# Performance work log

Hardware: AMD Instinct MI355X
Metric: run time of the kernel (lower is better)

The kernel has to match this reference:

```python
import jax, jax.numpy as jnp
import numpy as np

N_NODES = 100000
NUM_FEATURES = 64
HIDDEN = 128
OUT_CONV2 = 100


def gcn_conv(x, W, b, src, dst, n):
    """PyG GCNConv: add self-loops, symmetric degree norm, scatter-add."""
    x = x @ W  # [N, out]
    loop = jnp.arange(n, dtype=src.dtype)
    src2 = jnp.concatenate([src, loop])  # [E+N]
    dst2 = jnp.concatenate([dst, loop])
    deg = jax.ops.segment_sum(jnp.ones_like(dst2, dtype=x.dtype), dst2, num_segments=n)
    dinv = jnp.where(deg > 0, deg ** -0.5, 0.0)
    norm = dinv[src2] * dinv[dst2]  # [E+N]
    msg = x[src2] * norm[:, None]  # gather + scale
    out = jax.ops.segment_sum(msg, dst2, num_segments=n)  # scatter-add
    return out + b


def setup_inputs() -> dict:
    key = jax.random.key(0)
    ks = jax.random.split(key, 8)
    E = 1600000
    x = jax.random.normal(ks[0], (N_NODES, NUM_FEATURES), dtype=jnp.float32)
    edge_index = jax.random.randint(ks[1], (2, E), 0, N_NODES, dtype=jnp.int64)
    # Glorot-style init for GCNConv weights, zeros bias (PyG defaults)
    s1 = (6.0 / (NUM_FEATURES + HIDDEN)) ** 0.5
    W1 = jax.random.uniform(ks[2], (NUM_FEATURES, HIDDEN), minval=-s1, maxval=s1, dtype=jnp.float32)
    b1 = jnp.zeros((HIDDEN,), dtype=jnp.float32)
    s2 = (6.0 / (HIDDEN + OUT_CONV2)) ** 0.5
    W2 = jax.random.uniform(ks[3], (HIDDEN, OUT_CONV2), minval=-s2, maxval=s2, dtype=jnp.float32)
    b2 = jnp.zeros((OUT_CONV2,), dtype=jnp.float32)
    sl = (1.0 / OUT_CONV2) ** 0.5
    Wl = jax.random.uniform(ks[4], (OUT_CONV2, 1), minval=-sl, maxval=sl, dtype=jnp.float32)
    bl = jax.random.uniform(ks[5], (1,), minval=-sl, maxval=sl, dtype=jnp.float32)
    return {"x": x, "edge_index": edge_index, "W1": W1, "b1": b1,
            "W2": W2, "b2": b2, "Wl": Wl, "bl": bl}


def reference(x, edge_index, W1, b1, W2, b2, Wl, bl):
    src, dst = edge_index[0], edge_index[1]
    h = gcn_conv(x, W1, b1, src, dst, N_NODES)
    h = jax.nn.relu(h)
    # F.dropout with training=False (eval/inference) is identity
    h = gcn_conv(h, W2, b2, src, dst, N_NODES)
    return h @ Wl + bl  # [N, 1]
```

## Files before the change

### kernel.cpp

```cpp
#include <hip/hip_runtime.h>
#include <hip/hip_fp16.h>


#define N_NODES 100000
#define F_IN 64
#define HID 128
#define OUT2 100
#define BSHIFT 6
#define BNODES 64
#define NBUCKETS ((N_NODES + BNODES - 1) / BNODES)
#define SCAP 1408
#define ACHUNK 4096
#define NB_PAD 2048
#define SENTB 0xFFFFu
#define SENTE 0xFFFFFFFFu
#define TSHIFT 13
#define NTILES 13
#define RSTRIDE 77
#define ZROW N_NODES
#define YSCALE 4096.0f
#define YINV   (1.0f / 4096.0f)
#define ZSCALE 8192.0f
#define ZINV   (1.0f / 8192.0f)

typedef _Float16 half8 __attribute__((ext_vector_type(8)));
typedef float f32x4 __attribute__((ext_vector_type(4)));

static __device__ __forceinline__ half8 as_half8(uint4 u) {
    union { uint4 u; half8 h; } x; x.u = u; return x.h;
}

__global__ __launch_bounds__(256) void partA_kernel(
    const int* __restrict__ src, const int* __restrict__ dst,
    int* __restrict__ bcur, unsigned int* __restrict__ ebuf, int E, int nchunks,
    const float* __restrict__ W1, const float* __restrict__ W2,
    const float* __restrict__ b2, const float* __restrict__ Wl,
    const float* __restrict__ bl,
    float* __restrict__ v, float* __restrict__ c, uint4* __restrict__ Wpk,
    int* __restrict__ yzero) {
    int t = threadIdx.x;
    if ((int)blockIdx.x >= nchunks) {
        int pb = (int)blockIdx.x - nchunks;
        if (pb < 8) {
            int idx = pb * 256 + t;
            int lane2 = idx & 63;
            int kf    = (idx >> 6) & 1;
            int cb    = (idx >> 7) & 7;
            int part  = (idx >> 10) & 1;
            union { uint4 u; unsigned short s[8]; } pk;
            #pragma unroll
            for (int j = 0; j < 8; ++j) {
                int k    = kf * 32 + (lane2 >> 4) * 8 + j;
                int colg = cb * 16 + (lane2 & 15);
                float w = W1[k * HID + colg];
                __half h = __float2half_rn(w);
                if (part) h = __float2half_rn(w - __half2float(h));
                pk.s[j] = __half_as_ushort(h);
            }
            Wpk[idx] = pk.u;
        } else {
            if (t < HID) {
                float acc = 0.f;
                for (int k = 0; k < OUT2; ++k) acc += W2[t * OUT2 + k] * Wl[k];
                v[t] = acc;
            } else if (t == HID) {
                float acc = bl[0];
                for (int k = 0; k < OUT2; ++k) acc += b2[k] * Wl[k];
                *c = acc;
            }
            if (t < 128) yzero[t] = 0;
        }
        return;
    }
    __shared__ unsigned int stage[ACHUNK];
    __shared__ unsigned short sb[ACHUNK];
    __shared__ int hist[NB_PAD];
    __shared__ int ocnt[NB_PAD];
    __shared__ int gbase[NB_PAD];
    __shared__ int cnt2[NB_PAD];
    int base = blockIdx.x * ACHUNK;
    int total = E - base; if (total > ACHUNK) total = ACHUNK;

    #pragma unroll
    for (int i = 0; i < 8; ++i) { hist[t + i * 256] = 0; cnt2[t + i * 256] = 0; }
    __syncthreads();

    unsigned int pe[16];
    unsigned short bk[16];
    #pragma unroll
    for (int k = 0; k < 16; ++k) {
        int e = base + k * 256 + t;
        if (e < E) {
            int s = src[e], d = dst[e];
            pe[k] = ((unsigned int)s << BSHIFT) | (unsigned int)(d & (BNODES - 1));
            bk[k] = (unsigned short)(d >> BSHIFT);
            atomicAdd(&hist[bk[k]], 1);
        } else {
            bk[k] = SENTB;
        }
    }
    __syncthreads();
    #pragma unroll
    for (int i = 0; i < 8; ++i) ocnt[t + i * 256] = hist[t + i * 256];
    __syncthreads();
    for (int off = 1; off < NB_PAD; off <<= 1) {
        int v8[8];
        #pragma unroll
        for (int i = 0; i < 8; ++i) {
            int p = t + i * 256;
            v8[i] = (p >= off) ? hist[p - off] : 0;
        }
        __syncthreads();
        #pragma unroll
        for (int i = 0; i < 8; ++i) hist[t + i * 256] += v8[i];
        __syncthreads();
    }
    #pragma unroll
    for (int i = 0; i < 8; ++i) {
        int b = (t + i * 256 + blockIdx.x * 131) & (NB_PAD - 1);
        int cc = ocnt[b];
        if (cc > 0 && b < NBUCKETS)
            gbase[b] = b * SCAP + atomicAdd(&bcur[b], cc);
    }
    __syncthreads();
    #pragma unroll
    for (int k = 0; k < 16; ++k) {
        if (bk[k] != SENTB) {
            int b = bk[k];
            int pos = (hist[b] - ocnt[b]) + atomicAdd(&cnt2[b], 1);
            stage[pos] = pe[k];
            sb[pos] = (unsigned short)b;
        }
    }
    __syncthreads();
    #pragma unroll
    for (int k = 0; k < 16; ++k) {
        int idx = k * 256 + t;
        if (idx < total) {
            int b = sb[idx];
            int lo = hist[b] - ocnt[b];
            ebuf[gbase[b] + (idx - lo)] = stage[idx];
        }
    }
}

__global__ __launch_bounds__(256) void partB_kernel(
    const int* __restrict__ bcur, unsigned int* __restrict__ csr,
    float* __restrict__ dinv,
    const float4* __restrict__ x4, uint2* __restrict__ y2, int n) {
    __shared__ int lcnt[BNODES];
    __shared__ float sdinv[BNODES];
    __shared__ int tcnt[16];
    __shared__ int tcur[16];
    __shared__ unsigned int sbuf[SCAP];
    int b = blockIdx.x, t = threadIdx.x;
    int node0 = b << BSHIFT;
    int nlocal = min(BNODES, n - node0);
    int base = b * SCAP;
    int cnt = bcur[b];
    if (t < BNODES) lcnt[t] = 0;
    if (t < 16) tcnt[t] = 0;
    __syncthreads();
    unsigned int er[6];
    #pragma unroll
    for (int k = 0; k < 6; ++k) {
        int idx = k * 256 + t;
        er[k] = (idx < cnt) ? csr[base + idx] : SENTE;
        if (er[k] != SENTE) {
            atomicAdd(&lcnt[er[k] & (BNODES - 1)], 1);
            atomicAdd(&tcnt[er[k] >> (BSHIFT + TSHIFT)], 1);
        }
    }
    __syncthreads();
    if (t < BNODES) {
        float sd = rsqrtf((float)lcnt[t] + 1.0f);
        sdinv[t] = sd;
        if (t < nlocal) dinv[node0 + t] = sd;
    }
    if (t == 0) {
        int s = 0;
        #pragma unroll
        for (int i = 0; i < NTILES; ++i) { tcur[i] = s; s += tcnt[i]; }
    }
    __syncthreads();
    #pragma unroll
    for (int k = 0; k < 6; ++k) {
        unsigned int e = er[k];
        if (e != SENTE) {
            int p = atomicAdd(&tcur[e >> (BSHIFT + TSHIFT)], 1);
            sbuf[p] = e;
        }
    }
    __syncthreads();
    for (int idx = t; idx < cnt; idx += 256) csr[base + idx] = sbuf[idx];
    for (int i = t; i < nlocal * 16; i += 256) {
        int nl = i >> 4;
        int gi = (node0 + nl) * 16 + (i & 15);
        float sc = sdinv[nl] * YSCALE;
        float4 xv = x4[gi];
        int a0 = __float2int_rn(xv.x * sc);
        int a1 = __float2int_rn(xv.y * sc);
        int a2 = __float2int_rn(xv.z * sc);
        int a3 = __float2int_rn(xv.w * sc);
        uint2 pk;
        pk.x = ((unsigned int)a0 & 0xFFFFu) | ((unsigned int)a1 << 16);
        pk.y = ((unsigned int)a2 & 0xFFFFu) | ((unsigned int)a3 << 16);
        y2[gi] = pk;
    }
}

#define F1_ISSUE(EE, U, DL)                                            \
    _Pragma("unroll")                                                  \
    for (int g = 0; g < 8; ++g) {                                      \
        unsigned int e_ = __shfl((EE), g * 8 + q, 64);                 \
        int srow_ = (e_ != SENTE) ? (int)(e_ >> BSHIFT) : ZROW;        \
        DL[g] = (int)(e_ & (BNODES - 1));                              \
        U[g] = y4[srow_ * 8 + col];                                    \
    }

#define F1_CONSUME(U, DL)                                              \
    _Pragma("unroll")                                                  \
    for (int g = 0; g < 8; ++g) {                                      \
        int* rowp_ = &acci[DL[g] * RSTRIDE + col * 9];                 \
        const int* up_ = (const int*)&U[g];                            \
        _Pragma("unroll")                                              \
        for (int j = 0; j < 4; ++j) {                                  \
            int d_ = up_[j];                                           \
            atomicAdd(&rowp_[2 * j],     (d_ << 16) >> 16);            \
            atomicAdd(&rowp_[2 * j + 1], d_ >> 16);                    \
        }                                                              \
    }

__global__ __launch_bounds__(256, 6) void fused1_kernel(
    const int4* __restrict__ y4, const short* __restrict__ yh,
    const unsigned int* __restrict__ csr, const int* __restrict__ bcur,
    const float* __restrict__ dinv, const uint4* __restrict__ Wpk,
    const float* __restrict__ b1, const float* __restrict__ v,
    float* __restrict__ zz, int n) {
    __shared__ int acci[BNODES * RSTRIDE];
    int t = threadIdx.x;
    int lane = t & 63, wave = t >> 6;
    int q = lane >> 3, col = lane & 7;
    int b = blockIdx.x;
    int node0 = b << BSHIFT;
    int nlocal = min(BNODES, n - node0);
    int base = b * SCAP;
    int cnt = bcur[b];

    for (int r = wave; r < BNODES; r += 4) {
        int vv = 0;
        if (r < nlocal) vv = (int)yh[(node0 + r) * 64 + lane];
        acci[r * RSTRIDE + q * 9 + col] = vv;
    }
    __syncthreads();

    int nr = (cnt + 255) >> 8;
    int lpos = wave * 64 + lane;
    unsigned int ee = (lpos < cnt) ? csr[base + lpos] : SENTE;
    for (int r = 0; r < nr; ++r) {
        int pn = lpos + (r + 1) * 256;
        unsigned int een = (pn < cnt) ? csr[base + pn] : SENTE;
        int4 u[8]; int dl[8];
        F1_ISSUE(ee, u, dl);
        F1_CONSUME(u, dl);
        ee = een;
    }
    __syncthreads();

    int mm = lane & 15, kq = lane >> 4;
    int st = wave;
    int row = st * 16 + mm;
    float dis = ((row < nlocal) ? dinv[node0 + row] : 0.f) * YINV;
    const int* ap = &acci[row * RSTRIDE];
    half8 A0, A1;
    #pragma unroll
    for (int j = 0; j < 8; ++j) {
        A0[j] = (_Float16)(dis * (float)ap[kq * 9 + j]);
        A1[j] = (_Float16)(dis * (float)ap[(4 + kq) * 9 + j]);
    }
    f32x4 acc[8];
    #pragma unroll
    for (int cb = 0; cb < 8; ++cb) acc[cb] = (f32x4){0.f, 0.f, 0.f, 0.f};
    #pragma unroll
    for (int cb = 0; cb < 8; ++cb) {
        half8 bh0 = as_half8(Wpk[(cb * 2 + 0) * 64 + lane]);
        half8 bh1 = as_half8(Wpk[(cb * 2 + 1) * 64 + lane]);
        half8 bl0 = as_half8(Wpk[1024 + (cb * 2 + 0) * 64 + lane]);
        half8 bl1 = as_half8(Wpk[1024 + (cb * 2 + 1) * 64 + lane]);
        acc[cb] = __builtin_amdgcn_mfma_f32_16x16x32_f16(A0, bh0, acc[cb], 0, 0, 0);
        acc[cb] = __builtin_amdgcn_mfma_f32_16x16x32_f16(A1, bh1, acc[cb], 0, 0, 0);
        acc[cb] = __builtin_amdgcn_mfma_f32_16x16x32_f16(A0, bl0, acc[cb], 0, 0, 0);
        acc[cb] = __builtin_amdgcn_mfma_f32_16x16x32_f16(A1, bl1, acc[cb], 0, 0, 0);
    }
    float zp[4] = {0.f, 0.f, 0.f, 0.f};
    #pragma unroll
    for (int cb = 0; cb < 8; ++cb) {
        int colg = cb * 16 + mm;
        float bb1 = b1[colg], vv = v[colg];
        #pragma unroll
        for (int rr = 0; rr < 4; ++rr) {
            float h = acc[cb][rr] + bb1;
            h = fmaxf(h, 0.f);
            zp[rr] += h * vv;
        }
    }
    #pragma unroll
    for (int off = 1; off < 16; off <<= 1) {
        #pragma unroll
        for (int rr = 0; rr < 4; ++rr) zp[rr] += __shfl_xor(zp[rr], off, 64);
    }
    if (mm == 0) {
        int nb = st * 16 + kq * 4;
        #pragma unroll
        for (int rr = 0; rr < 4; ++rr)
            if (nb + rr < nlocal)
                zz[node0 + nb + rr] = dinv[node0 + nb + rr] * zp[rr];
    }
}

__global__ __launch_bounds__(256) void out_kernel(
    const int* __restrict__ bcur, const unsigned int* __restrict__ csr,
    const float* __restrict__ dinv, const float* __restrict__ zz,
    const float* __restrict__ c, float* __restrict__ out, int n) {
    __shared__ int acc2[BNODES];
    int b = blockIdx.x, t = threadIdx.x;
    int node0 = b << BSHIFT;
    int nlocal = min(BNODES, n - node0);
    int base = b * SCAP;
    int cnt = bcur[b];
    if (t < BNODES) acc2[t] = 0;
    __syncthreads();
    for (int idx = t; idx < cnt; idx += 256) {
        unsigned int e = csr[base + idx];
        float z = zz[e >> BSHIFT];
        atomicAdd(&acc2[e & (BNODES - 1)], __float2int_rn(z * ZSCALE));
    }
    __syncthreads();
    if (t < nlocal) {
        int node = node0 + t;
        out[node] = c[0] + dinv[node] * ((float)acc2[t] * ZINV + zz[node]);
    }
}

extern "C" void kernel_launch(void* const* d_in, const int* in_sizes, int n_in,
                              void* d_out, int out_size, void* d_ws, size_t ws_size,
                              hipStream_t stream) {
    const float* x  = (const float*)d_in[0];
    const int*   ei = (const int*)d_in[1];
    const float* W1 = (const float*)d_in[2];
    const float* b1 = (const float*)d_in[3];
    const float* W2 = (const float*)d_in[4];
    const float* b2 = (const float*)d_in[5];
    const float* Wl = (const float*)d_in[6];
    const float* bl = (const float*)d_in[7];
    float* out = (float*)d_out;

    int E = in_sizes[1] / 2;
    const int* src = ei;
    const int* dst = ei + E;

    float* ws      = (float*)d_ws;
    float* dinv    = ws;
    float* zz      = dinv + N_NODES;
    float* v       = zz + N_NODES;
    float* c       = v + HID;
    int*   bcur    = (int*)(c + 4);
    int*   csr     = bcur + NB_PAD;
    uint4* Wpk     = (uint4*)(csr + (size_t)NBUCKETS * SCAP);
    short* y       = (short*)((float*)Wpk + 8192);

    int nchunks = (E + ACHUNK - 1) / ACHUNK;

    hipMemsetAsync(bcur, 0, NBUCKETS * sizeof(int), stream);
    partA_kernel<<<nchunks + 9, 256, 0, stream>>>(
        src, dst, bcur, (unsigned int*)csr, E, nchunks,
        W1, W2, b2, Wl, bl, v, c, Wpk, (int*)(y + (size_t)ZROW * 64));
    partB_kernel<<<NBUCKETS, 256, 0, stream>>>(
        bcur, (unsigned int*)csr, dinv, (const float4*)x, (uint2*)y, N_NODES);
    fused1_kernel<<<NBUCKETS, 256, 0, stream>>>(
        (const int4*)y, (const short*)y, (const unsigned int*)csr,
        bcur, dinv, Wpk, b1, v, zz, N_NODES);
    out_kernel<<<NBUCKETS, 256, 0, stream>>>(
        bcur, (const unsigned int*)csr, dinv, zz, c, out, N_NODES);
}
```

Measured before the change: 179.2 us.

## Use two-level block scan in partA and sort edges by (tile, dst) in partB

```diff
diff --git a/kernel.cpp b/kernel.cpp
--- a/kernel.cpp
+++ b/kernel.cpp
@@ -16,6 +16,7 @@
 #define SENTE 0xFFFFFFFFu
 #define TSHIFT 13
 #define NTILES 13
+#define NKEY_PAD 1024
 #define RSTRIDE 77
 #define ZROW N_NODES
 #define YSCALE 4096.0f
@@ -78,6 +79,7 @@
     __shared__ int ocnt[NB_PAD];
     __shared__ int gbase[NB_PAD];
     __shared__ int cnt2[NB_PAD];
+    __shared__ int tsum[256];
     int base = blockIdx.x * ACHUNK;
     int total = E - base; if (total > ACHUNK) total = ACHUNK;
 
@@ -103,18 +105,22 @@
     #pragma unroll
     for (int i = 0; i < 8; ++i) ocnt[t + i * 256] = hist[t + i * 256];
     __syncthreads();
-    for (int off = 1; off < NB_PAD; off <<= 1) {
-        int v8[8];
-        #pragma unroll
-        for (int i = 0; i < 8; ++i) {
-            int p = t + i * 256;
-            v8[i] = (p >= off) ? hist[p - off] : 0;
-        }
+    int lcl[8];
+    int s = 0;
+    #pragma unroll
+    for (int i = 0; i < 8; ++i) { s += hist[8 * t + i]; lcl[i] = s; }
+    tsum[t] = s;
+    __syncthreads();
+    for (int off = 1; off < 256; off <<= 1) {
+        int vv = (t >= off) ? tsum[t - off] : 0;
         __syncthreads();
-        #pragma unroll
-        for (int i = 0; i < 8; ++i) hist[t + i * 256] += v8[i];
+        tsum[t] += vv;
         __syncthreads();
     }
+    int cbase = tsum[t] - s;
+    #pragma unroll
+    for (int i = 0; i < 8; ++i) hist[8 * t + i] = cbase + lcl[i];
+    __syncthreads();
     #pragma unroll
     for (int i = 0; i < 8; ++i) {
         int b = (t + i * 256 + blockIdx.x * 131) & (NB_PAD - 1);
@@ -148,18 +154,18 @@
     const int* __restrict__ bcur, unsigned int* __restrict__ csr,
     float* __restrict__ dinv,
     const float4* __restrict__ x4, uint2* __restrict__ y2, int n) {
-    __shared__ int lcnt[BNODES];
+    __shared__ int scnt[NKEY_PAD];
+    __shared__ int kbase[NKEY_PAD];
+    __shared__ int tsum[256];
     __shared__ float sdinv[BNODES];
-    __shared__ int tcnt[16];
-    __shared__ int tcur[16];
     __shared__ unsigned int sbuf[SCAP];
     int b = blockIdx.x, t = threadIdx.x;
     int node0 = b << BSHIFT;
     int nlocal = min(BNODES, n - node0);
     int base = b * SCAP;
     int cnt = bcur[b];
-    if (t < BNODES) lcnt[t] = 0;
-    if (t < 16) tcnt[t] = 0;
+    #pragma unroll
+    for (int i = 0; i < 4; ++i) scnt[t + i * 256] = 0;
     __syncthreads();
     unsigned int er[6];
     #pragma unroll
@@ -167,27 +173,41 @@
         int idx = k * 256 + t;
         er[k] = (idx < cnt) ? csr[base + idx] : SENTE;
         if (er[k] != SENTE) {
-            atomicAdd(&lcnt[er[k] & (BNODES - 1)], 1);
-            atomicAdd(&tcnt[er[k] >> (BSHIFT + TSHIFT)], 1);
+            int key = (int)((er[k] >> (BSHIFT + TSHIFT)) << 6) | (int)(er[k] & 63u);
+            atomicAdd(&scnt[key], 1);
         }
     }
     __syncthreads();
     if (t < BNODES) {
-        float sd = rsqrtf((float)lcnt[t] + 1.0f);
+        int deg = 0;
+        #pragma unroll
+        for (int i = 0; i < NTILES; ++i) deg += scnt[(i << 6) | t];
+        float sd = rsqrtf((float)deg + 1.0f);
         sdinv[t] = sd;
         if (t < nlocal) dinv[node0 + t] = sd;
     }
-    if (t == 0) {
-        int s = 0;
-        #pragma unroll
-        for (int i = 0; i < NTILES; ++i) { tcur[i] = s; s += tcnt[i]; }
-    }
+    int lcl[4];
+    int s = 0;
+    #pragma unroll
+    for (int i = 0; i < 4; ++i) { lcl[i] = s; s += scnt[4 * t + i]; }
+    tsum[t] = s;
+    __syncthreads();
+    for (int off = 1; off < 256; off <<= 1) {
+        int vv = (t >= off) ? tsum[t - off] : 0;
+        __syncthreads();
+        tsum[t] += vv;
+        __syncthreads();
+    }
+    int cbase = tsum[t] - s;
+    #pragma unroll
+    for (int i = 0; i < 4; ++i) kbase[4 * t + i] = cbase + lcl[i];
     __syncthreads();
     #pragma unroll
     for (int k = 0; k < 6; ++k) {
         unsigned int e = er[k];
         if (e != SENTE) {
-            int p = atomicAdd(&tcur[e >> (BSHIFT + TSHIFT)], 1);
+            int key = (int)((e >> (BSHIFT + TSHIFT)) << 6) | (int)(e & 63u);
+            int p = atomicAdd(&kbase[key], 1);
             sbuf[p] = e;
         }
     }
```

Result: no change. 182.4 us (+1.8%).

## Replace single-pass edge bucketing with two-level radix partition via superbuckets

Applied to the files above, without the earlier changes.

```diff
diff --git a/kernel.cpp b/kernel.cpp
--- a/kernel.cpp
+++ b/kernel.cpp
@@ -10,12 +10,13 @@
 #define BNODES 64
 #define NBUCKETS ((N_NODES + BNODES - 1) / BNODES)
 #define SCAP 1408
-#define ACHUNK 4096
+#define NSUPER 25
+#define SSHIFT 12
+#define SSCAP 66560
+#define SBKT 64
+#define ACH 4096
 #define NB_PAD 2048
-#define SENTB 0xFFFFu
 #define SENTE 0xFFFFFFFFu
-#define TSHIFT 13
-#define NTILES 13
 #define RSTRIDE 77
 #define ZROW N_NODES
 #define YSCALE 4096.0f
@@ -30,9 +31,9 @@
     union { uint4 u; half8 h; } x; x.u = u; return x.h;
 }
 
-__global__ __launch_bounds__(256) void partA_kernel(
+__global__ __launch_bounds__(256) void a1_kernel(
     const int* __restrict__ src, const int* __restrict__ dst,
-    int* __restrict__ bcur, unsigned int* __restrict__ ebuf, int E, int nchunks,
+    int* __restrict__ scur, unsigned int* __restrict__ sbuf1, int E, int nchunks,
     const float* __restrict__ W1, const float* __restrict__ W2,
     const float* __restrict__ b2, const float* __restrict__ Wl,
     const float* __restrict__ bl,
@@ -72,64 +73,48 @@
         }
         return;
     }
-    __shared__ unsigned int stage[ACHUNK];
-    __shared__ unsigned short sb[ACHUNK];
-    __shared__ int hist[NB_PAD];
-    __shared__ int ocnt[NB_PAD];
-    __shared__ int gbase[NB_PAD];
-    __shared__ int cnt2[NB_PAD];
-    int base = blockIdx.x * ACHUNK;
-    int total = E - base; if (total > ACHUNK) total = ACHUNK;
-
-    #pragma unroll
-    for (int i = 0; i < 8; ++i) { hist[t + i * 256] = 0; cnt2[t + i * 256] = 0; }
+    __shared__ unsigned int stage[ACH];
+    __shared__ unsigned char sb[ACH];
+    __shared__ int hist[32], lo[32], gbase[32], cnt2[32];
+    int base = blockIdx.x * ACH;
+    int total = E - base; if (total > ACH) total = ACH;
+
+    if (t < 32) { hist[t] = 0; cnt2[t] = 0; }
     __syncthreads();
 
     unsigned int pe[16];
-    unsigned short bk[16];
+    int bk[16];
     #pragma unroll
     for (int k = 0; k < 16; ++k) {
         int e = base + k * 256 + t;
         if (e < E) {
             int s = src[e], d = dst[e];
-            pe[k] = ((unsigned int)s << BSHIFT) | (unsigned int)(d & (BNODES - 1));
-            bk[k] = (unsigned short)(d >> BSHIFT);
+            pe[k] = ((unsigned int)s << 12) |
+                    ((unsigned int)((d >> BSHIFT) & 63) << 6) |
+                    (unsigned int)(d & 63);
+            bk[k] = d >> SSHIFT;
             atomicAdd(&hist[bk[k]], 1);
         } else {
-            bk[k] = SENTB;
-        }
-    }
-    __syncthreads();
-    #pragma unroll
-    for (int i = 0; i < 8; ++i) ocnt[t + i * 256] = hist[t + i * 256];
-    __syncthreads();
-    for (int off = 1; off < NB_PAD; off <<= 1) {
-        int v8[8];
+            bk[k] = -1;
+        }
+    }
+    __syncthreads();
+    if (t == 0) {
+        int run = 0;
         #pragma unroll
-        for (int i = 0; i < 8; ++i) {
-            int p = t + i * 256;
-            v8[i] = (p >= off) ? hist[p - off] : 0;
-        }
-        __syncthreads();
-        #pragma unroll
-        for (int i = 0; i < 8; ++i) hist[t + i * 256] += v8[i];
-        __syncthreads();
-    }
-    #pragma unroll
-    for (int i = 0; i < 8; ++i) {
-        int b = (t + i * 256 + blockIdx.x * 131) & (NB_PAD - 1);
-        int cc = ocnt[b];
-        if (cc > 0 && b < NBUCKETS)
-            gbase[b] = b * SCAP + atomicAdd(&bcur[b], cc);
-    }
-    __syncthreads();
-    #pragma unroll
-    for (int k = 0; k < 16; ++k) {
-        if (bk[k] != SENTB) {
+        for (int i = 0; i < NSUPER; ++i) { lo[i] = run; run += hist[i]; }
+    }
+    __syncthreads();
+    if (t < NSUPER && hist[t] > 0)
+        gbase[t] = t * SSCAP + atomicAdd(&scur[t], hist[t]);
+    __syncthreads();
+    #pragma unroll
+    for (int k = 0; k < 16; ++k) {
+        if (bk[k] >= 0) {
             int b = bk[k];
-            int pos = (hist[b] - ocnt[b]) + atomicAdd(&cnt2[b], 1);
+            int pos = lo[b] + atomicAdd(&cnt2[b], 1);
             stage[pos] = pe[k];
-            sb[pos] = (unsigned short)b;
+            sb[pos] = (unsigned char)b;
         }
     }
     __syncthreads();
@@ -138,61 +123,99 @@
         int idx = k * 256 + t;
         if (idx < total) {
             int b = sb[idx];
-            int lo = hist[b] - ocnt[b];
-            ebuf[gbase[b] + (idx - lo)] = stage[idx];
+            sbuf1[gbase[b] + (idx - lo[b])] = stage[idx];
+        }
+    }
+}
+
+__global__ __launch_bounds__(256) void a2_kernel(
+    const int* __restrict__ scur, const unsigned int* __restrict__ sbuf1,
+    int* __restrict__ bcur, unsigned int* __restrict__ csr) {
+    __shared__ unsigned int stage[ACH];
+    __shared__ unsigned char sb[ACH];
+    __shared__ int hist[SBKT], lo[SBKT], gbase[SBKT], cnt2[SBKT];
+    int t = threadIdx.x;
+    int sblk = blockIdx.x / 17;
+    int j = blockIdx.x % 17;
+    int cnt = scur[sblk]; if (cnt > SSCAP) cnt = SSCAP;
+    int start = j * ACH;
+    if (start >= cnt) return;
+    int total = cnt - start; if (total > ACH) total = ACH;
+    const unsigned int* sp = sbuf1 + (size_t)sblk * SSCAP + start;
+
+    if (t < SBKT) { hist[t] = 0; cnt2[t] = 0; }
+    __syncthreads();
+
+    unsigned int pe[16];
+    int bk[16];
+    #pragma unroll
+    for (int k = 0; k < 16; ++k) {
+        int idx = k * 256 + t;
+        if (idx < total) {
+            unsigned int w = sp[idx];
+            pe[k] = ((w >> 12) << 6) | (w & 63u);
+            bk[k] = (int)((w >> 6) & 63u);
+            atomicAdd(&hist[bk[k]], 1);
+        } else {
+            bk[k] = -1;
+        }
+    }
+    __syncthreads();
+    if (t == 0) {
+        int run = 0;
+        #pragma unroll
+        for (int i = 0; i < SBKT; ++i) { lo[i] = run; run += hist[i]; }
+    }
+    __syncthreads();
+    if (t < SBKT && hist[t] > 0) {
+        int bucket = sblk * SBKT + t;
+        if (bucket < NBUCKETS)
+            gbase[t] = bucket * SCAP + atomicAdd(&bcur[bucket], hist[t]);
+    }
+    __syncthreads();
+    #pragma unroll
+    for (int k = 0; k < 16; ++k) {
+        if (bk[k] >= 0) {
+            int b = bk[k];
+            int pos = lo[b] + atomicAdd(&cnt2[b], 1);
+            stage[pos] = pe[k];
+            sb[pos] = (unsigned char)b;
+        }
+    }
+    __syncthreads();
+    #pragma unroll
+    for (int k = 0; k < 16; ++k) {
+        int idx = k * 256 + t;
+        if (idx < total) {
+            int b = sb[idx];
+            csr[gbase[b] + (idx - lo[b])] = stage[idx];
         }
     }
 }
 
 __global__ __launch_bounds__(256) void partB_kernel(
-    const int* __restrict__ bcur, unsigned int* __restrict__ csr,
+    const int* __restrict__ bcur, const unsigned int* __restrict__ csr,
     float* __restrict__ dinv,
     const float4* __restrict__ x4, uint2* __restrict__ y2, int n) {
     __shared__ int lcnt[BNODES];
     __shared__ float sdinv[BNODES];
-    __shared__ int tcnt[16];
-    __shared__ int tcur[16];
-    __shared__ unsigned int sbuf[SCAP];
     int b = blockIdx.x, t = threadIdx.x;
     int node0 = b << BSHIFT;
     int nlocal = min(BNODES, n - node0);
     int base = b * SCAP;
     int cnt = bcur[b];
+    if (cnt > SCAP) cnt = SCAP;
     if (t < BNODES) lcnt[t] = 0;
-    if (t < 16) tcnt[t] = 0;
-    __syncthreads();
-    unsigned int er[6];
-    #pragma unroll
-    for (int k = 0; k < 6; ++k) {
-        int idx = k * 256 + t;
-        er[k] = (idx < cnt) ? csr[base + idx] : SENTE;
-        if (er[k] != SENTE) {
-            atomicAdd(&lcnt[er[k] & (BNODES - 1)], 1);
-            atomicAdd(&tcnt[er[k] >> (BSHIFT + TSHIFT)], 1);
-        }
-    }
+    __syncthreads();
+    for (int idx = t; idx < cnt; idx += 256)
+        atomicAdd(&lcnt[csr[base + idx] & (BNODES - 1)], 1);
     __syncthreads();
     if (t < BNODES) {
         float sd = rsqrtf((float)lcnt[t] + 1.0f);
         sdinv[t] = sd;
         if (t < nlocal) dinv[node0 + t] = sd;
     }
-    if (t == 0) {
-        int s = 0;
-        #pragma unroll
-        for (int i = 0; i < NTILES; ++i) { tcur[i] = s; s += tcnt[i]; }
-    }
-    __syncthreads();
-    #pragma unroll
-    for (int k = 0; k < 6; ++k) {
-        unsigned int e = er[k];
-        if (e != SENTE) {
-            int p = atomicAdd(&tcur[e >> (BSHIFT + TSHIFT)], 1);
-            sbuf[p] = e;
-        }
-    }
-    __syncthreads();
-    for (int idx = t; idx < cnt; idx += 256) csr[base + idx] = sbuf[idx];
+    __syncthreads();
     for (int i = t; i < nlocal * 16; i += 256) {
         int nl = i >> 4;
         int gi = (node0 + nl) * 16 + (i & 15);
@@ -246,6 +269,7 @@
     int nlocal = min(BNODES, n - node0);
     int base = b * SCAP;
     int cnt = bcur[b];
+    if (cnt > SCAP) cnt = SCAP;
 
     for (int r = wave; r < BNODES; r += 4) {
         int vv = 0;
@@ -328,6 +352,7 @@
     int nlocal = min(BNODES, n - node0);
     int base = b * SCAP;
     int cnt = bcur[b];
+    if (cnt > SCAP) cnt = SCAP;
     if (t < BNODES) acc2[t] = 0;
     __syncthreads();
     for (int idx = t; idx < cnt; idx += 256) {
@@ -360,23 +385,27 @@
     const int* dst = ei + E;
 
     float* ws      = (float*)d_ws;
-    float* dinv    = ws;
+    int*   scur    = (int*)ws;
+    int*   bcur    = scur + 32;
+    float* dinv    = (float*)(bcur + NB_PAD);
     float* zz      = dinv + N_NODES;
     float* v       = zz + N_NODES;
     float* c       = v + HID;
-    int*   bcur    = (int*)(c + 4);
-    int*   csr     = bcur + NB_PAD;
+    int*   csr     = (int*)(c + 4);
     uint4* Wpk     = (uint4*)(csr + (size_t)NBUCKETS * SCAP);
     short* y       = (short*)((float*)Wpk + 8192);
-
-    int nchunks = (E + ACHUNK - 1) / ACHUNK;
-
-    hipMemsetAsync(bcur, 0, NBUCKETS * sizeof(int), stream);
-    partA_kernel<<<nchunks + 9, 256, 0, stream>>>(
-        src, dst, bcur, (unsigned int*)csr, E, nchunks,
+    unsigned int* sbuf1 = (unsigned int*)y;
+
+    int nchunks = (E + ACH - 1) / ACH;
+
+    hipMemsetAsync(scur, 0, (32 + NB_PAD) * sizeof(int), stream);
+    a1_kernel<<<nchunks + 9, 256, 0, stream>>>(
+        src, dst, scur, sbuf1, E, nchunks,
         W1, W2, b2, Wl, bl, v, c, Wpk, (int*)(y + (size_t)ZROW * 64));
+    a2_kernel<<<NSUPER * 17, 256, 0, stream>>>(
+        scur, sbuf1, bcur, (unsigned int*)csr);
     partB_kernel<<<NBUCKETS, 256, 0, stream>>>(
-        bcur, (unsigned int*)csr, dinv, (const float4*)x, (uint2*)y, N_NODES);
+        bcur, (const unsigned int*)csr, dinv, (const float4*)x, (uint2*)y, N_NODES);
     fused1_kernel<<<NBUCKETS, 256, 0, stream>>>(
         (const int4*)y, (const short*)y, (const unsigned int*)csr,
         bcur, dinv, Wpk, b1, v, zz, N_NODES);
```

New measurement: 181.0 us. Within noise of the previous version (+1.0%).
